# Performance work log

Hardware: AMD Instinct MI355X
Metric: run time of the kernel (lower is better)

The kernel has to match this reference:

```python
import jax, jax.numpy as jnp
import numpy as np

DEPTH, DIM, HEADS, DIM_HEAD = 6, 1024, 16, 64
INNER = HEADS * DIM_HEAD  # 1024
DFF = 4 * DIM             # 4096
SCALE = DIM_HEAD ** -0.5


def setup_inputs() -> dict:
    key = jax.random.key(0)
    ks = jax.random.split(key, 12)
    def w(k, shape, fan_in):
        return jax.random.normal(k, shape, dtype=jnp.float32) * (fan_in ** -0.5)
    return {
        "x":     jax.random.normal(ks[0], (2, 2048, DIM), dtype=jnp.float32),
        "Wq":    w(ks[1], (DEPTH, DIM, INNER), DIM),
        "Wkv":   w(ks[2], (DEPTH, DIM, 2 * INNER), DIM),
        "Wo":    w(ks[3], (DEPTH, INNER, DIM), INNER),
        "bo":    jnp.zeros((DEPTH, DIM), dtype=jnp.float32),
        "ln1_g": jnp.ones((DEPTH, DIM), dtype=jnp.float32),
        "ln1_b": jnp.zeros((DEPTH, DIM), dtype=jnp.float32),
        "ln2_g": jnp.ones((DEPTH, DIM), dtype=jnp.float32),
        "ln2_b": jnp.zeros((DEPTH, DIM), dtype=jnp.float32),
        "W1":    w(ks[4], (DEPTH, DIM, DFF), DIM),
        "b1":    jnp.zeros((DEPTH, DFF), dtype=jnp.float32),
        "W2":    w(ks[5], (DEPTH, DFF, DIM), DFF),
        "b2":    jnp.zeros((DEPTH, DIM), dtype=jnp.float32),
    }


def _layernorm(x, g, b, eps=1e-5):
    mu = jnp.mean(x, axis=-1, keepdims=True)
    var = jnp.mean(jnp.square(x - mu), axis=-1, keepdims=True)
    return (x - mu) * jax.lax.rsqrt(var + eps) * g + b


def reference(x, Wq, Wkv, Wo, bo, ln1_g, ln1_b, ln2_g, ln2_b, W1, b1, W2, b2):
    b, n, _ = x.shape
    for l in range(DEPTH):
        # --- PreNorm self-attention ---
        h = _layernorm(x, ln1_g[l], ln1_b[l])
        q = h @ Wq[l]                       # [b, n, inner]
        kv = h @ Wkv[l]
        k, v = jnp.split(kv, 2, axis=-1)
        def heads(t):
            return t.reshape(b, n, HEADS, DIM_HEAD).transpose(0, 2, 1, 3)  # [b, h, n, d]
        q, k, v = heads(q), heads(k), heads(v)
        dots = jnp.einsum('bhid,bhjd->bhij', q, k) * SCALE
        attn = jax.nn.softmax(dots, axis=-1)
        out = jnp.einsum('bhij,bhjd->bhid', attn, v)
        out = out.transpose(0, 2, 1, 3).reshape(b, n, INNER)
        x = out @ Wo[l] + bo[l] + x
        # --- PreNorm feed-forward (exact GELU, matching torch nn.GELU default) ---
        h = _layernorm(x, ln2_g[l], ln2_b[l])
        h = jax.nn.gelu(h @ W1[l] + b1[l], approximate=False)
        x = h @ W2[l] + b2[l] + x
    return x
```

## Files before the change

### kernel.cpp

```cpp
#include <hip/hip_runtime.h>
#include <hip/hip_bf16.h>
#include <cstdint>
#include <cstddef>

#define DEPTH 6
#define DIM   1024
#define HEADS 16
#define DIMH  64
#define INNER 1024
#define DFF   4096
#define SEQ   2048
#define NTOK  4096

typedef __attribute__((ext_vector_type(8))) short bf16x8;
typedef __attribute__((ext_vector_type(4))) short bf16x4;
typedef __attribute__((ext_vector_type(4))) float f32x4;
typedef __hip_bfloat16 bf16;

#define CS 0.18033688011112042f
#define SMAX 24.0f

__device__ __forceinline__ void gld_lds16(const void* g, void* l) {
  __builtin_amdgcn_global_load_lds(
      (const __attribute__((address_space(1))) unsigned int*)g,
      (__attribute__((address_space(3))) unsigned int*)l,
      16, 0, 0);
}

__global__ __launch_bounds__(256) void transpose_convert(
    const float* __restrict__ in, bf16* __restrict__ out,
    int K, int N, int row0, int orows)
{
  __shared__ float tile[32][33];
  const int d  = blockIdx.z;
  const int n0 = blockIdx.x * 32, k0 = blockIdx.y * 32;
  const int c = threadIdx.x & 31, rb = threadIdx.x >> 5;
  const float* src = in + ((size_t)d * K + k0) * N + n0;
#pragma unroll
  for (int rr = 0; rr < 4; ++rr) {
    int r = rb + rr * 8;
    tile[r][c] = src[(size_t)r * N + c];
  }
  __syncthreads();
  bf16* dst = out + ((size_t)d * orows + row0 + n0) * K + k0;
#pragma unroll
  for (int rr = 0; rr < 4; ++rr) {
    int r = rb + rr * 8;
    dst[(size_t)r * K + c] = __float2bfloat16(tile[c][r]);
  }
}

__global__ __launch_bounds__(256) void ln_kernel(
    const float* __restrict__ x, const float* __restrict__ g,
    const float* __restrict__ b, bf16* __restrict__ h)
{
  const int row = blockIdx.x;
  const int tid = threadIdx.x;
  const float4 xv = *(const float4*)(x + (size_t)row * DIM + tid * 4);
  float s  = xv.x + xv.y + xv.z + xv.w;
  float s2 = xv.x * xv.x + xv.y * xv.y + xv.z * xv.z + xv.w * xv.w;
#pragma unroll
  for (int off = 1; off < 64; off <<= 1) {
    s  += __shfl_xor(s, off);
    s2 += __shfl_xor(s2, off);
  }
  __shared__ float red[8];
  const int wave = tid >> 6, lane = tid & 63;
  if (lane == 0) { red[wave * 2] = s; red[wave * 2 + 1] = s2; }
  __syncthreads();
  const float ts  = red[0] + red[2] + red[4] + red[6];
  const float ts2 = red[1] + red[3] + red[5] + red[7];
  const float mu  = ts * (1.0f / DIM);
  const float var = ts2 * (1.0f / DIM) - mu * mu;
  const float rstd = rsqrtf(var + 1e-5f);
  const float4 gv = *(const float4*)(g + tid * 4);
  const float4 bv = *(const float4*)(b + tid * 4);
  bf16 hv[4];
  hv[0] = __float2bfloat16((xv.x - mu) * rstd * gv.x + bv.x);
  hv[1] = __float2bfloat16((xv.y - mu) * rstd * gv.y + bv.y);
  hv[2] = __float2bfloat16((xv.z - mu) * rstd * gv.z + bv.z);
  hv[3] = __float2bfloat16((xv.w - mu) * rstd * gv.w + bv.w);
  *(uint2*)(h + (size_t)row * DIM + tid * 4) = *(uint2*)hv;
}

template<int EPI, bool SWZ, int BN>
__global__ __launch_bounds__(256) void gemm_t(
    const bf16* __restrict__ A, const bf16* __restrict__ Bt,
    int N, int K,
    const float* __restrict__ bias,
    float* __restrict__ outf, bf16* __restrict__ outb,
    bf16* __restrict__ outq, bf16* __restrict__ outk, bf16* __restrict__ outvt)
{
  constexpr int NW = BN / 32;
  __shared__ alignas(16) bf16 As[128 * 64];
  __shared__ alignas(16) bf16 Bs[BN * 64];
  const int tid  = threadIdx.x;
  const int lane = tid & 63;
  const int wave = tid >> 6;
  const int wr = wave >> 1, wc = wave & 1;

  int bx, by;
  if (SWZ) {
    const int gx   = (int)gridDim.x;
    const int nwg  = gx * (int)gridDim.y;
    const int wg   = blockIdx.x + blockIdx.y * gx;
    const int xcd  = wg & 7;
    const int slot = wg >> 3;
    const int id   = xcd * (nwg >> 3) + slot;
    by = id / gx;
    bx = id % gx;
  } else {
    bx = blockIdx.x; by = blockIdx.y;
  }
  const int m0 = by * 128, n0 = bx * BN;
  const int sr = tid >> 3, pc = tid & 7;
  const int wbase = (tid & ~63) << 4;

  f32x4 acc[4][NW];
#pragma unroll
  for (int m = 0; m < 4; ++m)
#pragma unroll
    for (int n = 0; n < NW; ++n) acc[m][n] = (f32x4){0.f, 0.f, 0.f, 0.f};

  for (int k0 = 0; k0 < K; k0 += 64) {
#pragma unroll
    for (int it = 0; it < 4; ++it) {
      const int r  = it * 32 + sr;
      const int lc = pc ^ (r & 7);
      gld_lds16(A + (size_t)(m0 + r) * K + k0 + lc * 8, (char*)As + it * 4096 + wbase);
    }
#pragma unroll
    for (int it = 0; it < NW; ++it) {
      const int r  = it * 32 + sr;
      const int lc = pc ^ (r & 7);
      gld_lds16(Bt + (size_t)(n0 + r) * K + k0 + lc * 8, (char*)Bs + it * 4096 + wbase);
    }
    __syncthreads();
#pragma unroll
    for (int kk = 0; kk < 2; ++kk) {
      const int cb = kk * 4 + (lane >> 4);
      bf16x8 af[4], bfr[NW];
#pragma unroll
      for (int m = 0; m < 4; ++m) {
        const int r = wr * 64 + m * 16 + (lane & 15);
        af[m] = *(const bf16x8*)((const char*)As + r * 128 + ((cb ^ (r & 7)) << 4));
      }
#pragma unroll
      for (int n = 0; n < NW; ++n) {
        const int r = wc * (BN / 2) + n * 16 + (lane & 15);
        bfr[n] = *(const bf16x8*)((const char*)Bs + r * 128 + ((cb ^ (r & 7)) << 4));
      }
#pragma unroll
      for (int m = 0; m < 4; ++m)
#pragma unroll
        for (int n = 0; n < NW; ++n)
          acc[m][n] = __builtin_amdgcn_mfma_f32_16x16x32_bf16(af[m], bfr[n], acc[m][n], 0, 0, 0);
    }
    __syncthreads();
  }

#pragma unroll
  for (int m = 0; m < 4; ++m) {
    const int rb = m0 + wr * 64 + m * 16 + ((lane >> 4) << 2);
#pragma unroll
    for (int n = 0; n < NW; ++n) {
      const int col = n0 + wc * (BN / 2) + n * 16 + (lane & 15);
      if (EPI == 0 && col >= 2048) {
        const int batch = rb >> 11, tok = rb & 2047;
        const int c = col - 2048;
        union { bf16x4 v4; short s[4]; } w;
#pragma unroll
        for (int j = 0; j < 4; ++j) {
          const bf16 bb = __float2bfloat16(acc[m][n][j]);
          w.s[j] = *(const short*)&bb;
        }
        *(bf16x4*)(outvt + (((size_t)(batch * HEADS + (c >> 6))) * DIMH + (c & 63)) * SEQ + tok)
            = w.v4;
        continue;
      }
#pragma unroll
      for (int j = 0; j < 4; ++j) {
        const int row = rb + j;
        const float v = acc[m][n][j];
        if (EPI == 0) {
          const int batch = row >> 11, tok = row & 2047;
          if (col < 1024) {
            outq[(((size_t)(batch * HEADS + (col >> 6))) * SEQ + tok) * DIMH + (col & 63)] =
                __float2bfloat16(v * CS);
          } else {
            const int c = col - 1024;
            outk[(((size_t)(batch * HEADS + (c >> 6))) * SEQ + tok) * DIMH + (c & 63)] =
                __float2bfloat16(v);
          }
        } else if (EPI == 1) {
          const size_t off = (size_t)row * N + col;
          outf[off] = v + bias[col] + outf[off];
        } else if (EPI == 2) {
          const float t = v + bias[col];
          const float gg = 0.5f * t * (1.0f + erff(t * 0.70710678118654752f));
          outb[(size_t)row * N + col] = __float2bfloat16(gg);
        }
      }
    }
  }
}

__global__ __launch_bounds__(256) void attn_kernel(
    const bf16* __restrict__ q, const bf16* __restrict__ k,
    const bf16* __restrict__ vt, bf16* __restrict__ out)
{
  __shared__ alignas(16) bf16 Ks[2][2][64 * 64];
  __shared__ alignas(16) bf16 Vs[2][2][64 * 64];
  const int tid  = threadIdx.x;
  const int lane = tid & 63;
  const int wave = tid >> 6;
  const int g    = lane >> 4;
  const int lm   = lane & 15;
  const int bh   = blockIdx.y;
  const int qw   = blockIdx.x * 128 + wave * 32;
  const int sr = tid >> 3, pc = tid & 7;
  const int wbase = (tid & ~63) << 4;

  bf16x8 qf[2][2];
#pragma unroll
  for (int m = 0; m < 2; ++m)
#pragma unroll
    for (int kk = 0; kk < 2; ++kk)
      qf[m][kk] = *(const bf16x8*)(q + ((size_t)bh * SEQ + qw + m * 16 + lm) * DIMH
                                   + kk * 32 + g * 8);

  f32x4 ao[2][4];
#pragma unroll
  for (int m = 0; m < 2; ++m)
#pragma unroll
    for (int n = 0; n < 4; ++n) ao[m][n] = (f32x4){0.f, 0.f, 0.f, 0.f};
  float lrow[2] = {0.f, 0.f};

  auto stage = [&](int jt2, int buf) {
#pragma unroll
    for (int sub = 0; sub < 2; ++sub) {
      const int jt = jt2 * 2 + sub;
#pragma unroll
      for (int it = 0; it < 2; ++it) {
        const int r  = it * 32 + sr;
        const int lc = pc ^ (r & 7);
        gld_lds16(k  + ((size_t)bh * SEQ + jt * 64 + r) * DIMH + lc * 8,
                  (char*)&Ks[buf][sub][0] + it * 4096 + wbase);
        gld_lds16(vt + ((size_t)bh * DIMH + r) * SEQ + jt * 64 + lc * 8,
                  (char*)&Vs[buf][sub][0] + it * 4096 + wbase);
      }
    }
  };

  stage(0, 0);
  __syncthreads();

  for (int jt2 = 0; jt2 < SEQ / 128; ++jt2) {
    const int buf = jt2 & 1;
    const bool pref = (jt2 + 1 < SEQ / 128);
    if (pref) {
      stage(jt2 + 1, buf ^ 1);
      asm volatile("s_waitcnt vmcnt(8)" ::: "memory");
    } else {
      asm volatile("s_waitcnt vmcnt(0)" ::: "memory");
    }

#pragma unroll
    for (int sub = 0; sub < 2; ++sub) {
      f32x4 sa[2][4];
#pragma unroll
      for (int m = 0; m < 2; ++m)
#pragma unroll
        for (int n = 0; n < 4; ++n)
          sa[m][n] = (f32x4){-SMAX, -SMAX, -SMAX, -SMAX};
      __builtin_amdgcn_s_setprio(1);
#pragma unroll
      for (int kk = 0; kk < 2; ++kk)
#pragma unroll
        for (int n = 0; n < 4; ++n) {
          const int row = n * 16 + lm;
          const bf16x8 af = *(const bf16x8*)((const char*)&Ks[buf][sub][0] + row * 128
                                             + (((kk * 4 + g) ^ (row & 7)) << 4));
#pragma unroll
          for (int m = 0; m < 2; ++m)
            sa[m][n] = __builtin_amdgcn_mfma_f32_16x16x32_bf16(af, qf[m][kk], sa[m][n], 0, 0, 0);
        }
      __builtin_amdgcn_s_setprio(0);

      bf16x8 pa[2][2];
#pragma unroll
      for (int m = 0; m < 2; ++m) {
        float rs = 0.f;
#pragma unroll
        for (int n = 0; n < 4; ++n)
#pragma unroll
          for (int r = 0; r < 4; ++r) {
            const float p = exp2f(sa[m][n][r]);
            sa[m][n][r] = p;
            rs += p;
          }
        rs += __shfl_xor(rs, 16);
        rs += __shfl_xor(rs, 32);
        lrow[m] += rs;
#pragma unroll
        for (int h = 0; h < 2; ++h) {
          union { bf16x8 v8; short s[8]; } u;
#pragma unroll
          for (int n2 = 0; n2 < 2; ++n2)
#pragma unroll
            for (int r = 0; r < 4; ++r) {
              const bf16 bb = __float2bfloat16(sa[m][h * 2 + n2][r]);
              u.s[n2 * 4 + r] = *(const short*)&bb;
            }
          pa[m][h] = u.v8;
        }
      }

      __builtin_amdgcn_s_setprio(1);
#pragma unroll
      for (int n = 0; n < 4; ++n) {
        const int row = n * 16 + lm;
        const char* vb = (const char*)&Vs[buf][sub][0] + row * 128;
        const int sw = row & 7;
#pragma unroll
        for (int kk = 0; kk < 2; ++kk) {
          const bf16x4 lo = *(const bf16x4*)(vb + (((kk * 4 + (g >> 1)) ^ sw) << 4) + (g & 1) * 8);
          const bf16x4 hi = *(const bf16x4*)(vb + (((kk * 4 + 2 + (g >> 1)) ^ sw) << 4) + (g & 1) * 8);
          const bf16x8 vf = __builtin_shufflevector(lo, hi, 0, 1, 2, 3, 4, 5, 6, 7);
#pragma unroll
          for (int m = 0; m < 2; ++m)
            ao[m][n] = __builtin_amdgcn_mfma_f32_16x16x32_bf16(vf, pa[m][kk], ao[m][n], 0, 0, 0);
        }
      }
      __builtin_amdgcn_s_setprio(0);
    }
    __builtin_amdgcn_s_barrier();
  }

  const int batch = bh >> 4, head = bh & 15;
#pragma unroll
  for (int m = 0; m < 2; ++m) {
    const float linv = 1.0f / lrow[m];
    const int row = qw + m * 16 + lm;
    bf16* orow = out + ((size_t)batch * SEQ + row) * INNER + head * DIMH;
#pragma unroll
    for (int n = 0; n < 4; ++n) {
      union { bf16x4 v4; short s[4]; } w;
#pragma unroll
      for (int r = 0; r < 4; ++r) {
        const bf16 bb = __float2bfloat16(ao[m][n][r] * linv);
        w.s[r] = *(const short*)&bb;
      }
      *(bf16x4*)(orow + n * 16 + g * 4) = w.v4;
    }
  }
}

extern "C" void kernel_launch(void* const* d_in, const int* in_sizes, int n_in,
                              void* d_out, int out_size, void* d_ws, size_t ws_size,
                              hipStream_t stream)
{
  (void)in_sizes; (void)n_in; (void)out_size; (void)ws_size;
  const float* x_in = (const float*)d_in[0];
  const float* Wq   = (const float*)d_in[1];
  const float* Wkv  = (const float*)d_in[2];
  const float* Wo   = (const float*)d_in[3];
  const float* bo   = (const float*)d_in[4];
  const float* ln1g = (const float*)d_in[5];
  const float* ln1b = (const float*)d_in[6];
  const float* ln2g = (const float*)d_in[7];
  const float* ln2b = (const float*)d_in[8];
  const float* W1   = (const float*)d_in[9];
  const float* b1   = (const float*)d_in[10];
  const float* W2   = (const float*)d_in[11];
  const float* b2   = (const float*)d_in[12];
  float* xb = (float*)d_out;

  char* ws = (char*)d_ws;
  size_t off = 0;
  auto take = [&](size_t bytes) {
    char* p = ws + off;
    off += (bytes + 255) & ~(size_t)255;
    return p;
  };
  bf16* Wqkvt = (bf16*)take((size_t)DEPTH * 3072 * 1024 * 2);
  bf16* Wot   = (bf16*)take((size_t)DEPTH * 1024 * 1024 * 2);
  bf16* W1t   = (bf16*)take((size_t)DEPTH * 4096 * 1024 * 2);
  bf16* W2t   = (bf16*)take((size_t)DEPTH * 1024 * 4096 * 2);
  bf16* hb    = (bf16*)take((size_t)NTOK * DIM * 2);
  bf16* qbuf  = (bf16*)take((size_t)NTOK * INNER * 2);
  bf16* kbuf  = (bf16*)take((size_t)NTOK * INNER * 2);
  bf16* vtbuf = (bf16*)take((size_t)NTOK * INNER * 2);
  bf16* aobuf = (bf16*)take((size_t)NTOK * INNER * 2);
  bf16* h1buf = (bf16*)take((size_t)NTOK * DFF * 2);

  hipMemcpyAsync(xb, x_in, (size_t)NTOK * DIM * 4, hipMemcpyDeviceToDevice, stream);

  dim3 b256(256);
  transpose_convert<<<dim3(32, 32, DEPTH),  b256, 0, stream>>>(Wq,  Wqkvt, 1024, 1024, 0,    3072);
  transpose_convert<<<dim3(64, 32, DEPTH),  b256, 0, stream>>>(Wkv, Wqkvt, 1024, 2048, 1024, 3072);
  transpose_convert<<<dim3(32, 32, DEPTH),  b256, 0, stream>>>(Wo,  Wot,   1024, 1024, 0,    1024);
  transpose_convert<<<dim3(128, 32, DEPTH), b256, 0, stream>>>(W1,  W1t,   1024, 4096, 0,    4096);
  transpose_convert<<<dim3(32, 128, DEPTH), b256, 0, stream>>>(W2,  W2t,   4096, 1024, 0,    1024);

  for (int l = 0; l < DEPTH; ++l) {
    ln_kernel<<<NTOK, b256, 0, stream>>>(xb, ln1g + l * DIM, ln1b + l * DIM, hb);
    gemm_t<0, true, 128><<<dim3(3072 / 128, NTOK / 128), b256, 0, stream>>>(
        hb, Wqkvt + (size_t)l * 3072 * 1024, 3072, 1024,
        nullptr, nullptr, nullptr, qbuf, kbuf, vtbuf);
    attn_kernel<<<dim3(SEQ / 128, 32), b256, 0, stream>>>(qbuf, kbuf, vtbuf, aobuf);
    gemm_t<1, true, 64><<<dim3(1024 / 64, NTOK / 128), b256, 0, stream>>>(
        aobuf, Wot + (size_t)l * 1024 * 1024, 1024, 1024,
        bo + l * DIM, xb, nullptr, nullptr, nullptr, nullptr);
    ln_kernel<<<NTOK, b256, 0, stream>>>(xb, ln2g + l * DIM, ln2b + l * DIM, hb);
    gemm_t<2, true, 128><<<dim3(4096 / 128, NTOK / 128), b256, 0, stream>>>(
        hb, W1t + (size_t)l * 4096 * 1024, 4096, 1024,
        b1 + l * DFF, nullptr, h1buf, nullptr, nullptr, nullptr);
    gemm_t<1, true, 64><<<dim3(1024 / 64, NTOK / 128), b256, 0, stream>>>(
        h1buf, W2t + (size_t)l * 1024 * 4096, 1024, 4096,
        b2 + l * DIM, xb, nullptr, nullptr, nullptr, nullptr);
  }
}
```

Baseline: 1.700 ms.

## Add 256x128-tile 512-thread triple-buffered GEMM for QKV and FFN1

Adds a new GEMM kernel that uses a 256x128 output tile with 8 waves and a three-stage LDS pipeline driven by explicit vmcnt waits and barriers. MFMA blocks are wrapped in s_setprio. It replaces the 128x128 gemm_t for the QKV projection and the first FFN matmul. The larger tile raises operand reuse per block and the deeper prefetch hides more load latency, at the cost of roughly 144KB of LDS per block and fewer resident blocks. gemm_t is trimmed to keep only the EPI 1 and 2 epilogues.

```diff
diff --git a/kernel.cpp b/kernel.cpp
--- a/kernel.cpp
+++ b/kernel.cpp
@@ -165,6 +165,130 @@
 #pragma unroll
     for (int n = 0; n < NW; ++n) {
       const int col = n0 + wc * (BN / 2) + n * 16 + (lane & 15);
+#pragma unroll
+      for (int j = 0; j < 4; ++j) {
+        const int row = rb + j;
+        const float v = acc[m][n][j];
+        if (EPI == 1) {
+          const size_t off = (size_t)row * N + col;
+          outf[off] = v + bias[col] + outf[off];
+        } else if (EPI == 2) {
+          const float t = v + bias[col];
+          const float gg = 0.5f * t * (1.0f + erff(t * 0.70710678118654752f));
+          outb[(size_t)row * N + col] = __float2bfloat16(gg);
+        }
+      }
+    }
+  }
+}
+
+template<int EPI, bool SWZ>
+__global__ __launch_bounds__(512) void gemm256(
+    const bf16* __restrict__ A, const bf16* __restrict__ Bt,
+    int N, int K,
+    const float* __restrict__ bias,
+    float* __restrict__ outf, bf16* __restrict__ outb,
+    bf16* __restrict__ outq, bf16* __restrict__ outk, bf16* __restrict__ outvt)
+{
+  __shared__ alignas(16) bf16 As[3][256 * 64];
+  __shared__ alignas(16) bf16 Bs[3][128 * 64];
+  const int tid  = threadIdx.x;
+  const int lane = tid & 63;
+  const int wave = tid >> 6;
+  const int wr = wave >> 1;
+  const int wc = wave & 1;
+
+  int bx, by;
+  if (SWZ) {
+    const int gx   = (int)gridDim.x;
+    const int nwg  = gx * (int)gridDim.y;
+    const int wg   = blockIdx.x + blockIdx.y * gx;
+    const int xcd  = wg & 7;
+    const int slot = wg >> 3;
+    const int id   = xcd * (nwg >> 3) + slot;
+    by = id / gx;
+    bx = id % gx;
+  } else {
+    bx = blockIdx.x; by = blockIdx.y;
+  }
+  const int m0 = by * 256, n0 = bx * 128;
+  const int sr = tid >> 3, pc = tid & 7;
+
+  f32x4 acc[4][4];
+#pragma unroll
+  for (int m = 0; m < 4; ++m)
+#pragma unroll
+    for (int n = 0; n < 4; ++n) acc[m][n] = (f32x4){0.f, 0.f, 0.f, 0.f};
+
+  auto stage = [&](int kt, int b) {
+    const int k0 = kt << 6;
+#pragma unroll
+    for (int it = 0; it < 4; ++it) {
+      const int r  = it * 64 + sr;
+      const int lc = pc ^ (sr & 7);
+      gld_lds16(A + (size_t)(m0 + r) * K + k0 + lc * 8,
+                (char*)&As[b][0] + it * 8192 + tid * 16);
+    }
+#pragma unroll
+    for (int it = 0; it < 2; ++it) {
+      const int r  = it * 64 + sr;
+      const int lc = pc ^ (sr & 7);
+      gld_lds16(Bt + (size_t)(n0 + r) * K + k0 + lc * 8,
+                (char*)&Bs[b][0] + it * 8192 + tid * 16);
+    }
+  };
+
+  auto compute = [&](int b) {
+#pragma unroll
+    for (int kk = 0; kk < 2; ++kk) {
+      const int cb = kk * 4 + (lane >> 4);
+      bf16x8 af[4], bfr[4];
+#pragma unroll
+      for (int m = 0; m < 4; ++m) {
+        const int r = wr * 64 + m * 16 + (lane & 15);
+        af[m] = *(const bf16x8*)((const char*)&As[b][0] + r * 128 + ((cb ^ (r & 7)) << 4));
+      }
+#pragma unroll
+      for (int n = 0; n < 4; ++n) {
+        const int r = wc * 64 + n * 16 + (lane & 15);
+        bfr[n] = *(const bf16x8*)((const char*)&Bs[b][0] + r * 128 + ((cb ^ (r & 7)) << 4));
+      }
+      __builtin_amdgcn_s_setprio(1);
+#pragma unroll
+      for (int m = 0; m < 4; ++m)
+#pragma unroll
+        for (int n = 0; n < 4; ++n)
+          acc[m][n] = __builtin_amdgcn_mfma_f32_16x16x32_bf16(af[m], bfr[n], acc[m][n], 0, 0, 0);
+      __builtin_amdgcn_s_setprio(0);
+    }
+  };
+
+  const int nt = K >> 6;
+  stage(0, 0);
+  stage(1, 1);
+  asm volatile("s_waitcnt vmcnt(6)" ::: "memory");
+  __builtin_amdgcn_s_barrier();
+  int cur = 0;
+  for (int t = 0; t < nt; ++t) {
+    const int nxt2 = (cur + 2 >= 3) ? cur - 1 : cur + 2;
+    if (t + 2 < nt) {
+      stage(t + 2, nxt2);
+      compute(cur);
+      asm volatile("s_waitcnt vmcnt(6)" ::: "memory");
+    } else {
+      compute(cur);
+      asm volatile("s_waitcnt vmcnt(0)" ::: "memory");
+    }
+    __builtin_amdgcn_s_barrier();
+    cur = (cur + 1 == 3) ? 0 : cur + 1;
+  }
+
+#pragma unroll
+  for (int m = 0; m < 4; ++m) {
+    const int rb = m0 + wr * 64 + m * 16 + ((lane >> 4) << 2);
+#pragma unroll
+    for (int n = 0; n < 4; ++n) {
+      const int col = n0 + wc * 64 + n * 16 + (lane & 15);
       if (EPI == 0 && col >= 2048) {
         const int batch = rb >> 11, tok = rb & 2047;
         const int c = col - 2048;
@@ -192,9 +316,6 @@
             outk[(((size_t)(batch * HEADS + (c >> 6))) * SEQ + tok) * DIMH + (c & 63)] =
                 __float2bfloat16(v);
           }
-        } else if (EPI == 1) {
-          const size_t off = (size_t)row * N + col;
-          outf[off] = v + bias[col] + outf[off];
         } else if (EPI == 2) {
           const float t = v + bias[col];
           const float gg = 0.5f * t * (1.0f + erff(t * 0.70710678118654752f));
@@ -397,6 +518,7 @@
   hipMemcpyAsync(xb, x_in, (size_t)NTOK * DIM * 4, hipMemcpyDeviceToDevice, stream);
 
   dim3 b256(256);
+  dim3 b512(512);
   transpose_convert<<<dim3(32, 32, DEPTH),  b256, 0, stream>>>(Wq,  Wqkvt, 1024, 1024, 0,    3072);
   transpose_convert<<<dim3(64, 32, DEPTH),  b256, 0, stream>>>(Wkv, Wqkvt, 1024, 2048, 1024, 3072);
   transpose_convert<<<dim3(32, 32, DEPTH),  b256, 0, stream>>>(Wo,  Wot,   1024, 1024, 0,    1024);
@@ -405,7 +527,7 @@
 
   for (int l = 0; l < DEPTH; ++l) {
     ln_kernel<<<NTOK, b256, 0, stream>>>(xb, ln1g + l * DIM, ln1b + l * DIM, hb);
-    gemm_t<0, true, 128><<<dim3(3072 / 128, NTOK / 128), b256, 0, stream>>>(
+    gemm256<0, true><<<dim3(3072 / 128, NTOK / 256), b512, 0, stream>>>(
         hb, Wqkvt + (size_t)l * 3072 * 1024, 3072, 1024,
         nullptr, nullptr, nullptr, qbuf, kbuf, vtbuf);
     attn_kernel<<<dim3(SEQ / 128, 32), b256, 0, stream>>>(qbuf, kbuf, vtbuf, aobuf);
@@ -413,7 +535,7 @@
         aobuf, Wot + (size_t)l * 1024 * 1024, 1024, 1024,
         bo + l * DIM, xb, nullptr, nullptr, nullptr, nullptr);
     ln_kernel<<<NTOK, b256, 0, stream>>>(xb, ln2g + l * DIM, ln2b + l * DIM, hb);
-    gemm_t<2, true, 128><<<dim3(4096 / 128, NTOK / 128), b256, 0, stream>>>(
+    gemm256<2, true><<<dim3(4096 / 128, NTOK / 256), b512, 0, stream>>>(
         hb, W1t + (size_t)l * 4096 * 1024, 4096, 1024,
         b1 + l * DFF, nullptr, h1buf, nullptr, nullptr, nullptr);
     gemm_t<1, true, 64><<<dim3(1024 / 64, NTOK / 128), b256, 0, stream>>>(
```

Result: slower. 1.908 ms (+12.2%).
